# Kernel optimization log

Measured on AMD Instinct MI355X. Metric: run time of the kernel, lower is better.

## Reference

```python
import jax, jax.numpy as jnp
import numpy as np

DEPTH = 2; C = 96; DIN = 192; R = 6; N = 16; K = 4
B = 1; H0 = 64; W0 = 64; L0 = H0 * W0


def layer_norm(x, g, b, eps=1e-5):
    m = jnp.mean(x, -1, keepdims=True)
    v = jnp.var(x, -1, keepdims=True)
    return (x - m) / jnp.sqrt(v + eps) * g + b


def selective_scan(u, delta, A, Bs, Cs, D):
    # u, delta: (B, KD, L); A: (KD, N); Bs, Cs: (B, K, N, L); D: (KD,)
    Bb, KD, L = u.shape
    Kk = Bs.shape[1]; Dd = KD // Kk; Nn = A.shape[1]
    dA = jnp.exp(delta[..., None] * A[None, :, None, :])              # (B,KD,L,N)
    Bfull = jnp.broadcast_to(Bs[:, :, None], (Bb, Kk, Dd, Nn, L)).reshape(Bb, KD, Nn, L)
    Cfull = jnp.broadcast_to(Cs[:, :, None], (Bb, Kk, Dd, Nn, L)).reshape(Bb, KD, Nn, L)
    dBu = delta[..., None] * Bfull.transpose(0, 1, 3, 2) * u[..., None]  # (B,KD,L,N)
    Ct = Cfull.transpose(3, 0, 1, 2)                                   # (L,B,KD,N)

    def step(h, inp):
        dA_t, dBu_t, C_t = inp
        h = dA_t * h + dBu_t
        return h, jnp.sum(h * C_t, -1)

    init = jnp.zeros((Bb, KD, Nn), u.dtype)
    _, ys = jax.lax.scan(step, init, (dA.transpose(2, 0, 1, 3), dBu.transpose(2, 0, 1, 3), Ct))
    y = ys.transpose(1, 2, 0)                                          # (B,KD,L)
    return y + D[None, :, None] * u


def ss2d(x, in_proj_w, conv_w, conv_b, x_proj_w, dt_w, dt_b, A_logs, Ds, outn_g, outn_b, out_proj_w):
    # x: (B,H,W,C)
    Bb, H, W, Cc = x.shape
    L = H * W
    xz = x @ in_proj_w.T                                  # (B,H,W,2*DIN)
    Din = xz.shape[-1] // 2
    xc, z = xz[..., :Din], xz[..., Din:]
    xc = xc.transpose(0, 3, 1, 2)                         # (B,DIN,H,W)
    xc = jax.lax.conv_general_dilated(xc, conv_w, (1, 1), 'SAME',
                                      feature_group_count=Din,
                                      dimension_numbers=('NCHW', 'OIHW', 'NCHW'))
    xc = jax.nn.silu(xc + conv_b[None, :, None, None])
    # cross-scan: 4 directions
    x0 = xc.reshape(Bb, Din, L)
    x1 = xc.transpose(0, 1, 3, 2).reshape(Bb, Din, L)
    xs = jnp.stack([x0, x1, jnp.flip(x0, -1), jnp.flip(x1, -1)], 1)  # (B,K,DIN,L)
    x_dbl = jnp.einsum('bkdl,kcd->bkcl', xs, x_proj_w)
    dts, Bm, Cm = x_dbl[:, :, :R], x_dbl[:, :, R:R + N], x_dbl[:, :, R + N:]
    dts = jnp.einsum('bkrl,kdr->bkdl', dts, dt_w)
    u = xs.reshape(Bb, K * Din, L)
    delta = jax.nn.softplus(dts.reshape(Bb, K * Din, L) + dt_b.reshape(K * Din)[None, :, None])
    A = -jnp.exp(A_logs)                                  # (K*DIN, N)
    ys = selective_scan(u, delta, A, Bm, Cm, Ds).reshape(Bb, K, Din, L)
    # cross-merge
    y0 = ys[:, 0]
    y1 = ys[:, 1].reshape(Bb, Din, W, H).transpose(0, 1, 3, 2).reshape(Bb, Din, L)
    y2 = jnp.flip(ys[:, 2], -1)
    y3 = jnp.flip(ys[:, 3], -1).reshape(Bb, Din, W, H).transpose(0, 1, 3, 2).reshape(Bb, Din, L)
    y = (y0 + y1 + y2 + y3).transpose(0, 2, 1).reshape(Bb, H, W, Din)
    y = layer_norm(y, outn_g, outn_b)
    y = y * jax.nn.silu(z)
    return y @ out_proj_w.T                               # (B,H,W,C)


def setup_inputs() -> dict:
    key = jax.random.key(0)
    ks = jax.random.split(key, 10)
    f = jnp.float32
    rn = lambda k, s: jax.random.normal(k, s, f) * 0.02
    return {
        'x': jax.random.normal(ks[0], (B, L0, C), f),
        'H': H0, 'W': W0,
        'norm1_g': jnp.ones((DEPTH, C), f), 'norm1_b': jnp.zeros((DEPTH, C), f),
        'vssn_g': jnp.ones((DEPTH, C), f), 'vssn_b': jnp.zeros((DEPTH, C), f),
        'in_proj_w': rn(ks[1], (DEPTH, 2 * DIN, C)),
        'conv_w': rn(ks[2], (DEPTH, DIN, 1, 3, 3)),
        'conv_b': jnp.zeros((DEPTH, DIN), f),
        'x_proj_w': rn(ks[3], (DEPTH, K, R + 2 * N, DIN)),
        'dt_w': rn(ks[4], (DEPTH, K, DIN, R)),
        'dt_b': jax.random.uniform(ks[5], (DEPTH, K, DIN), f, -4.0, -2.0),
        'A_logs': jnp.log(jnp.broadcast_to(jnp.arange(1, N + 1, dtype=f), (DEPTH, K * DIN, N))),
        'Ds': jnp.ones((DEPTH, K * DIN), f),
        'outn_g': jnp.ones((DEPTH, DIN), f), 'outn_b': jnp.zeros((DEPTH, DIN), f),
        'out_proj_w': rn(ks[6], (DEPTH, C, DIN)),
        'res_conv_w': rn(ks[7], (C, C, 3, 3)),
        'res_conv_b': jnp.zeros((C,), f),
    }


def reference(x, H, W, norm1_g, norm1_b, vssn_g, vssn_b, in_proj_w, conv_w, conv_b,
              x_proj_w, dt_w, dt_b, A_logs, Ds, outn_g, outn_b, out_proj_w,
              res_conv_w, res_conv_b):
    Bb, Ll, Cc = x.shape
    shortcut = x
    for i in range(DEPTH):
        sc = x
        xn = layer_norm(x, norm1_g[i], norm1_b[i]).reshape(Bb, H, W, Cc)
        # VSSBlock: internal pre-norm + residual around SS2D (drop_path = 0)
        xi = xn + ss2d(layer_norm(xn, vssn_g[i], vssn_b[i]), in_proj_w[i], conv_w[i],
                       conv_b[i], x_proj_w[i], dt_w[i], dt_b[i], A_logs[i], Ds[i],
                       outn_g[i], outn_b[i], out_proj_w[i])
        x = sc + xi.reshape(Bb, Ll, Cc)
    xc = x.transpose(0, 2, 1).reshape(Bb, Cc, H, W)
    xc = jax.lax.conv_general_dilated(xc, res_conv_w, (1, 1), 'SAME',
                                      dimension_numbers=('NCHW', 'OIHW', 'NCHW'))
    xc = xc + res_conv_b[None, :, None, None]
    return xc.reshape(Bb, Cc, Ll).transpose(0, 2, 1) + shortcut
```

## Files before the change

kernel.cpp:

```cpp
#include <hip/hip_runtime.h>
#include <math.h>

#define LTOK 4096
#define CCH  96
#define DIN_ 192
#define KDIR 4
#define NST  16
#define KD_  768

#define O_XN     0
#define O_XZ     786432
#define O_XCONV  2359296
#define O_XCONVT 3145728
#define O_DELTA  3932160
#define O_BM     7077888
#define O_CM     7340032
#define O_YS     9961472
#define O_XCUR   13107200

__device__ __forceinline__ float siluf(float x) { return x / (1.f + __expf(-x)); }

__global__ void fusedA_kernel(const float* __restrict__ x, const float* __restrict__ g1,
                              const float* __restrict__ b1, const float* __restrict__ g2,
                              const float* __restrict__ b2, const float* __restrict__ w,
                              float* __restrict__ xn, float* __restrict__ xz) {
  __shared__ float As[96 * 72];
  __shared__ float Bs[96 * 68];
  int tid = threadIdx.x;
  int l0 = blockIdx.x * 64;
  int j0 = blockIdx.y * 64;
  int m = tid >> 2, j = tid & 3;
  int l = l0 + m;
  float v[24];
  float s = 0.f, ss = 0.f;
#pragma unroll
  for (int t = 0; t < 24; ++t) {
    int k = j + 4 * t;
    float vv = x[l * 96 + k];
    v[t] = vv; s += vv; ss += vv * vv;
  }
  s += __shfl_xor(s, 1); ss += __shfl_xor(ss, 1);
  s += __shfl_xor(s, 2); ss += __shfl_xor(ss, 2);
  float m1 = s * (1.f / 96.f);
  float rs1 = rsqrtf(ss * (1.f / 96.f) - m1 * m1 + 1e-5f);
  float s2 = 0.f, ss2 = 0.f;
#pragma unroll
  for (int t = 0; t < 24; ++t) {
    int k = j + 4 * t;
    float nv = (v[t] - m1) * rs1 * g1[k] + b1[k];
    v[t] = nv; s2 += nv; ss2 += nv * nv;
    if (blockIdx.y == 0) xn[l * 96 + k] = nv;
  }
  s2 += __shfl_xor(s2, 1); ss2 += __shfl_xor(ss2, 1);
  s2 += __shfl_xor(s2, 2); ss2 += __shfl_xor(ss2, 2);
  float m2 = s2 * (1.f / 96.f);
  float rs2 = rsqrtf(ss2 * (1.f / 96.f) - m2 * m2 + 1e-5f);
#pragma unroll
  for (int t = 0; t < 24; ++t) {
    int k = j + 4 * t;
    As[k * 72 + m] = (v[t] - m2) * rs2 * g2[k] + b2[k];
  }
  for (int qi = tid; qi < 64 * 24; qi += 256) {
    int nn = qi / 24, q = qi % 24;
    const float4 wv = *(const float4*)&w[(j0 + nn) * 96 + q * 4];
    Bs[(q * 4 + 0) * 68 + nn] = wv.x;
    Bs[(q * 4 + 1) * 68 + nn] = wv.y;
    Bs[(q * 4 + 2) * 68 + nn] = wv.z;
    Bs[(q * 4 + 3) * 68 + nn] = wv.w;
  }
  __syncthreads();
  int mg = tid & 15, ng = tid >> 4;
  float acc[4][4] = {};
  for (int k = 0; k < 96; ++k) {
    float a0 = As[k * 72 + 4 * mg + 0], a1 = As[k * 72 + 4 * mg + 1];
    float a2 = As[k * 72 + 4 * mg + 2], a3 = As[k * 72 + 4 * mg + 3];
    float b0 = Bs[k * 68 + 4 * ng + 0], b1_ = Bs[k * 68 + 4 * ng + 1];
    float b2_ = Bs[k * 68 + 4 * ng + 2], b3 = Bs[k * 68 + 4 * ng + 3];
    acc[0][0] += a0 * b0; acc[0][1] += a0 * b1_; acc[0][2] += a0 * b2_; acc[0][3] += a0 * b3;
    acc[1][0] += a1 * b0; acc[1][1] += a1 * b1_; acc[1][2] += a1 * b2_; acc[1][3] += a1 * b3;
    acc[2][0] += a2 * b0; acc[2][1] += a2 * b1_; acc[2][2] += a2 * b2_; acc[2][3] += a2 * b3;
    acc[3][0] += a3 * b0; acc[3][1] += a3 * b1_; acc[3][2] += a3 * b2_; acc[3][3] += a3 * b3;
  }
#pragma unroll
  for (int i = 0; i < 4; ++i) {
    float4 o = make_float4(acc[i][0], acc[i][1], acc[i][2], acc[i][3]);
    *(float4*)&xz[(l0 + 4 * mg + i) * 384 + j0 + 4 * ng] = o;
  }
}

__global__ void dwconvT_kernel(const float* __restrict__ xz, const float* __restrict__ cw,
                               const float* __restrict__ cb, float* __restrict__ xconv,
                               float* __restrict__ xconvT) {
  int w0 = blockIdx.x * 16, h0 = blockIdx.y * 16, d0 = blockIdx.z * 8;
  __shared__ float xs[324 * 9];
  int tid = threadIdx.x;
  for (int idx = tid; idx < 324 * 8; idx += 256) {
    int dd = idx & 7;
    int p = idx >> 3;
    int ph = p / 18, pw = p - ph * 18;
    int hh = h0 + ph - 1, ww = w0 + pw - 1;
    float v = 0.f;
    if (hh >= 0 && hh < 64 && ww >= 0 && ww < 64) v = xz[(hh * 64 + ww) * 384 + d0 + dd];
    xs[p * 9 + dd] = v;
  }
  __syncthreads();
  int wi = tid & 15, hi = tid >> 4;
  for (int dd = 0; dd < 8; ++dd) {
    int d = d0 + dd;
    float acc = cb[d];
    const float* wgt = cw + d * 9;
#pragma unroll
    for (int r = 0; r < 3; ++r)
#pragma unroll
      for (int c = 0; c < 3; ++c)
        acc += xs[((hi + r) * 18 + wi + c) * 9 + dd] * wgt[r * 3 + c];
    float o = siluf(acc);
    xconv[d * LTOK + (h0 + hi) * 64 + w0 + wi] = o;
    xconvT[d * LTOK + (w0 + wi) * 64 + h0 + hi] = o;
  }
}

__global__ __launch_bounds__(256) void projdelta_kernel(
    const float* __restrict__ xconv, const float* __restrict__ xconvT,
    const float* __restrict__ xpw, const float* __restrict__ dtw,
    const float* __restrict__ dtb, float* __restrict__ delta,
    float* __restrict__ Bm, float* __restrict__ Cm) {
  int chunk = blockIdx.x;
  int k = blockIdx.y;
  int l0 = chunk * 32;
  bool rev = (k >= 2);
  int lnat0 = rev ? (4064 - l0) : l0;
  const float* ub = ((k & 1) ? xconvT : xconv);
  __shared__ float Us[192 * 34];
  __shared__ float Ws[38 * 196];
  __shared__ float xdm[6 * 34];
  int tid = threadIdx.x;
  for (int idx = tid; idx < 192 * 8; idx += 256) {
    int q = idx & 7, d = idx >> 3;
    float4 v = *(const float4*)&ub[d * LTOK + lnat0 + 4 * q];
    *(float4*)&Us[d * 34 + 4 * q] = v;
  }
  for (int idx = tid; idx < 38 * 48; idx += 256) {
    int q = idx % 48, c = idx / 48;
    float4 v = *(const float4*)&xpw[(k * 38 + c) * 192 + 4 * q];
    *(float4*)&Ws[c * 196 + 4 * q] = v;
  }
  __syncthreads();
  int ip = tid & 31;
  int cg = tid >> 5;
  int crow[5];
#pragma unroll
  for (int j = 0; j < 5; ++j) {
    int c = cg * 5 + j;
    crow[j] = ((c < 38) ? c : 0) * 196;
  }
  float acc[5] = {};
  for (int d = 0; d < 192; d += 4) {
    float u0 = Us[(d + 0) * 34 + ip];
    float u1 = Us[(d + 1) * 34 + ip];
    float u2 = Us[(d + 2) * 34 + ip];
    float u3 = Us[(d + 3) * 34 + ip];
#pragma unroll
    for (int j = 0; j < 5; ++j) {
      const float4 wv = *(const float4*)&Ws[crow[j] + d];
      acc[j] += u0 * wv.x + u1 * wv.y + u2 * wv.z + u3 * wv.w;
    }
  }
  int i = rev ? (31 - ip) : ip;
  int l = l0 + i;
#pragma unroll
  for (int j = 0; j < 5; ++j) {
    int c = cg * 5 + j;
    if (c < 6)       xdm[c * 34 + ip] = acc[j];
    else if (c < 22) Bm[((k << 12) + l) * NST + (c - 6)] = acc[j];
    else if (c < 38) Cm[((k << 12) + l) * NST + (c - 22)] = acc[j];
  }
  __syncthreads();
  const float* dtwk = dtw + k * 192 * 6;
  const float* dtbk = dtb + k * 192;
  int dg = tid >> 5;
  for (int m = 0; m < 24; ++m) {
    int d = dg + 8 * m;
    float a = dtbk[d];
#pragma unroll
    for (int r = 0; r < 6; ++r) a += dtwk[d * 6 + r] * xdm[r * 34 + ip];
    float sp = (a > 20.f) ? a : log1pf(__expf(a));
    delta[(k * 192 + d) * LTOK + l] = sp;
  }
}

__global__ __launch_bounds__(512) void scan_fused(
    const float* __restrict__ delta, const float* __restrict__ Bm,
    const float* __restrict__ Cm, const float* __restrict__ xconv,
    const float* __restrict__ xconvT, const float* __restrict__ A_logs,
    const float* __restrict__ Ds, float* __restrict__ ys) {
  int kd = blockIdx.x;
  int k = kd / 192, d = kd - k * 192;
  int tid = threadIdx.x;
  int nq = tid & 3;
  int c = tid >> 2;
  const float* ub = ((k & 1) ? xconvT : xconv) + d * LTOK;
  bool rev = (k >= 2);
  float A0 = -__expf(A_logs[kd * 16 + 4 * nq + 0]);
  float A1 = -__expf(A_logs[kd * 16 + 4 * nq + 1]);
  float A2 = -__expf(A_logs[kd * 16 + 4 * nq + 2]);
  float A3 = -__expf(A_logs[kd * 16 + 4 * nq + 3]);
  const float* dp = delta + kd * LTOK;
  const float* bp = Bm + k * LTOK * NST;
  const float* cp = Cm + k * LTOK * NST;
  __shared__ float Ps[16 * 132], Qs[16 * 132], H0s[16 * 132];
  int l0 = c * 32;
  float h0 = 0.f, h1 = 0.f, h2 = 0.f, h3 = 0.f;
  float P0 = 1.f, P1 = 1.f, P2 = 1.f, P3 = 1.f;
  for (int t = 0; t < 32; t += 4) {
    int l = l0 + t;
    float4 dlt4 = *(const float4*)(dp + l);
    float4 u4;
    if (!rev) u4 = *(const float4*)(ub + l);
    else { float4 tp = *(const float4*)(ub + 4092 - l); u4 = make_float4(tp.w, tp.z, tp.y, tp.x); }
#pragma unroll
    for (int s = 0; s < 4; ++s) {
      float dlt = (s == 0) ? dlt4.x : (s == 1) ? dlt4.y : (s == 2) ? dlt4.z : dlt4.w;
      float uu  = (s == 0) ? u4.x  : (s == 1) ? u4.y  : (s == 2) ? u4.z  : u4.w;
      float4 B4 = *(const float4*)(bp + (l + s) * NST + 4 * nq);
      float du = dlt * uu;
      float a0 = __expf(dlt * A0), a1 = __expf(dlt * A1);
      float a2 = __expf(dlt * A2), a3 = __expf(dlt * A3);
      h0 = a0 * h0 + du * B4.x; h1 = a1 * h1 + du * B4.y;
      h2 = a2 * h2 + du * B4.z; h3 = a3 * h3 + du * B4.w;
      P0 *= a0; P1 *= a1; P2 *= a2; P3 *= a3;
    }
  }
  Ps[(4 * nq + 0) * 132 + c] = P0; Qs[(4 * nq + 0) * 132 + c] = h0;
  Ps[(4 * nq + 1) * 132 + c] = P1; Qs[(4 * nq + 1) * 132 + c] = h1;
  Ps[(4 * nq + 2) * 132 + c] = P2; Qs[(4 * nq + 2) * 132 + c] = h2;
  Ps[(4 * nq + 3) * 132 + c] = P3; Qs[(4 * nq + 3) * 132 + c] = h3;
  __syncthreads();
  {
    int wv = tid >> 6, lane = tid & 63;
#pragma unroll
    for (int r = 0; r < 2; ++r) {
      int nn = wv * 2 + r;
      float P = Ps[nn * 132 + lane];
      float S = Qs[nn * 132 + lane];
#pragma unroll
      for (int off = 1; off < 64; off <<= 1) {
        float pp = __shfl_up(P, off);
        float sp = __shfl_up(S, off);
        if (lane >= off) { S = sp * P + S; P = pp * P; }
      }
      float g0 = __shfl_up(S, 1);
      if (lane == 0) g0 = 0.f;
      H0s[nn * 132 + lane] = g0;
      float T0 = __shfl(S, 63);
      float P1_ = Ps[nn * 132 + 64 + lane];
      float S1_ = Qs[nn * 132 + 64 + lane];
#pragma unroll
      for (int off = 1; off < 64; off <<= 1) {
        float pp = __shfl_up(P1_, off);
        float sp = __shfl_up(S1_, off);
        if (lane >= off) { S1_ = sp * P1_ + S1_; P1_ = pp * P1_; }
      }
      float gex = __shfl_up(S1_, 1);
      float pex = __shfl_up(P1_, 1);
      if (lane == 0) { gex = 0.f; pex = 1.f; }
      H0s[nn * 132 + 64 + lane] = pex * T0 + gex;
    }
  }
  __syncthreads();
  float Dv = Ds[kd];
  float* yk = ys + (k * DIN_ + d) * LTOK;
  h0 = H0s[(4 * nq + 0) * 132 + c];
  h1 = H0s[(4 * nq + 1) * 132 + c];
  h2 = H0s[(4 * nq + 2) * 132 + c];
  h3 = H0s[(4 * nq + 3) * 132 + c];
  int row1 = 32 * (c & 1);
  int col1 = c >> 1;
  for (int t = 0; t < 32; t += 4) {
    int l = l0 + t;
    float4 dlt4 = *(const float4*)(dp + l);
    float4 u4;
    if (!rev) u4 = *(const float4*)(ub + l);
    else { float4 tp = *(const float4*)(ub + 4092 - l); u4 = make_float4(tp.w, tp.z, tp.y, tp.x); }
    float y4[4];
#pragma unroll
    for (int s = 0; s < 4; ++s) {
      float dlt = (s == 0) ? dlt4.x : (s == 1) ? dlt4.y : (s == 2) ? dlt4.z : dlt4.w;
      float uu  = (s == 0) ? u4.x  : (s == 1) ? u4.y  : (s == 2) ? u4.z  : u4.w;
      float4 B4 = *(const float4*)(bp + (l + s) * NST + 4 * nq);
      float4 C4 = *(const float4*)(cp + (l + s) * NST + 4 * nq);
      float du = dlt * uu;
      float a0 = __expf(dlt * A0), a1 = __expf(dlt * A1);
      float a2 = __expf(dlt * A2), a3 = __expf(dlt * A3);
      h0 = a0 * h0 + du * B4.x; h1 = a1 * h1 + du * B4.y;
      h2 = a2 * h2 + du * B4.z; h3 = a3 * h3 + du * B4.w;
      float p = h0 * C4.x + h1 * C4.y + h2 * C4.z + h3 * C4.w;
      p += __shfl_xor(p, 1);
      p += __shfl_xor(p, 2);
      y4[s] = p + Dv * uu;
    }
    if (nq == 0) {
      if (k == 0) {
        *(float4*)(yk + l) = make_float4(y4[0], y4[1], y4[2], y4[3]);
      } else if (k == 2) {
        *(float4*)(yk + 4092 - l) = make_float4(y4[3], y4[2], y4[1], y4[0]);
      } else if (k == 1) {
#pragma unroll
        for (int s = 0; s < 4; ++s) yk[(row1 + t + s) * 64 + col1] = y4[s];
      } else {
#pragma unroll
        for (int s = 0; s < 4; ++s) yk[(63 - row1 - (t + s)) * 64 + (63 - col1)] = y4[s];
      }
    }
  }
}

__global__ void combine_out(const float* __restrict__ ys, const float* __restrict__ xz,
                            const float* __restrict__ xn, const float* __restrict__ xsrc,
                            const float* __restrict__ og, const float* __restrict__ ob,
                            const float* __restrict__ ow, float* __restrict__ xout) {
  __shared__ float Ys[192 * 33];
  __shared__ float Bs[64 * 100];
  int tid = threadIdx.x;
  int l0 = blockIdx.x * 32;
  for (int it = tid; it < 192 * 8; it += 256) {
    int d = it >> 3, g = it & 7;
    int l = l0 + g * 4;
    float4 a0 = *(const float4*)&ys[(0 * DIN_ + d) * LTOK + l];
    float4 a1 = *(const float4*)&ys[(1 * DIN_ + d) * LTOK + l];
    float4 a2 = *(const float4*)&ys[(2 * DIN_ + d) * LTOK + l];
    float4 a3 = *(const float4*)&ys[(3 * DIN_ + d) * LTOK + l];
    float* yr = &Ys[d * 33 + g * 4];
    yr[0] = a0.x + a1.x + a2.x + a3.x;
    yr[1] = a0.y + a1.y + a2.y + a3.y;
    yr[2] = a0.z + a1.z + a2.z + a3.z;
    yr[3] = a0.w + a1.w + a2.w + a3.w;
  }
  __syncthreads();
  {
    int m = tid >> 3, q = tid & 7;
    int l = l0 + m;
    float zval[24];
    const float* zp = xz + l * 384 + 192 + q * 24;
#pragma unroll
    for (int i = 0; i < 6; ++i) {
      float4 zv = *(const float4*)(zp + 4 * i);
      zval[4 * i + 0] = zv.x; zval[4 * i + 1] = zv.y;
      zval[4 * i + 2] = zv.z; zval[4 * i + 3] = zv.w;
    }
    float s = 0.f, ssum = 0.f;
    float vv[24];
#pragma unroll
    for (int i = 0; i < 24; ++i) {
      float v = Ys[(q * 24 + i) * 33 + m];
      vv[i] = v; s += v; ssum += v * v;
    }
    s += __shfl_xor(s, 1); ssum += __shfl_xor(ssum, 1);
    s += __shfl_xor(s, 2); ssum += __shfl_xor(ssum, 2);
    s += __shfl_xor(s, 4); ssum += __shfl_xor(ssum, 4);
    float mu = s * (1.f / 192.f);
    float rs = rsqrtf(ssum * (1.f / 192.f) - mu * mu + 1e-5f);
#pragma unroll
    for (int i = 0; i < 24; ++i) {
      int d = q * 24 + i;
      float yn = (vv[i] - mu) * rs * og[d] + ob[d];
      Ys[d * 33 + m] = yn * siluf(zval[i]);
    }
  }
  int mg = tid & 31, cg = tid >> 5;
  float acc[12] = {};
  for (int kc = 0; kc < 3; ++kc) {
    __syncthreads();
    for (int qi = tid; qi < 96 * 16; qi += 256) {
      int cix = qi / 16, q = qi % 16;
      const float4 wv = *(const float4*)&ow[cix * 192 + kc * 64 + q * 4];
      Bs[(q * 4 + 0) * 100 + cix] = wv.x;
      Bs[(q * 4 + 1) * 100 + cix] = wv.y;
      Bs[(q * 4 + 2) * 100 + cix] = wv.z;
      Bs[(q * 4 + 3) * 100 + cix] = wv.w;
    }
    __syncthreads();
    for (int kk = 0; kk < 64; ++kk) {
      float a = Ys[(kc * 64 + kk) * 33 + mg];
      const float* br = &Bs[kk * 100 + cg * 12];
#pragma unroll
      for (int jj = 0; jj < 12; ++jj) acc[jj] += a * br[jj];
    }
  }
  int ll = l0 + mg;
#pragma unroll
  for (int jj = 0; jj < 12; ++jj) {
    int cix = cg * 12 + jj;
    xout[ll * 96 + cix] = xsrc[ll * 96 + cix] + xn[ll * 96 + cix] + acc[jj];
  }
}

__global__ void resconv_part(const float* __restrict__ x, const float* __restrict__ w,
                             float* __restrict__ pbuf) {
  int tile = blockIdx.x;
  int cs = blockIdx.y;
  int th0 = (tile >> 3) * 8, tw0 = (tile & 7) * 8;
  int cbase = cs * 6;
  __shared__ float xs[600];
  __shared__ float wlds[96 * 6 * 12];
  int tid = threadIdx.x;
  for (int idx = tid; idx < 600; idx += 256) {
    int cc = idx % 6;
    int pos = idx / 6;
    int hh = th0 + pos / 10 - 1;
    int ww = tw0 + pos % 10 - 1;
    float v = 0.f;
    if (hh >= 0 && hh < 64 && ww >= 0 && ww < 64) v = x[(hh * 64 + ww) * 96 + cbase + cc];
    xs[cc * 100 + pos] = v;
  }
  for (int idx = tid; idx < 96 * 54; idx += 256) {
    int c0 = idx / 54, o = idx - c0 * 54;
    int cc = o / 9, t = o - cc * 9;
    wlds[(c0 * 6 + cc) * 12 + t] = w[c0 * 864 + (cbase + cc) * 9 + t];
  }
  __syncthreads();
  int lane = tid & 63;
  int th = lane >> 3, tw = lane & 7;
  int c0g = tid >> 6;
  float acc[24] = {};
  for (int cc = 0; cc < 6; ++cc) {
    float xv[9];
#pragma unroll
    for (int r = 0; r < 3; ++r)
#pragma unroll
      for (int q = 0; q < 3; ++q) xv[r * 3 + q] = xs[cc * 100 + (th + r) * 10 + tw + q];
#pragma unroll
    for (int j = 0; j < 24; ++j) {
      const float* wr = &wlds[((c0g * 24 + j) * 6 + cc) * 12];
      float4 w0 = *(const float4*)wr;
      float4 w1 = *(const float4*)(wr + 4);
      float w8 = wr[8];
      acc[j] += xv[0] * w0.x + xv[1] * w0.y + xv[2] * w0.z + xv[3] * w0.w
              + xv[4] * w1.x + xv[5] * w1.y + xv[6] * w1.z + xv[7] * w1.w + xv[8] * w8;
    }
  }
  int l = (th0 + th) * 64 + tw0 + tw;
  float* pb = pbuf + cs * 393216 + l * 96 + c0g * 24;
#pragma unroll
  for (int j = 0; j < 24; j += 4)
    *(float4*)(pb + j) = make_float4(acc[j], acc[j + 1], acc[j + 2], acc[j + 3]);
}

__global__ void resconv_reduce(const float* __restrict__ pbuf, const float* __restrict__ b,
                               const float* __restrict__ shortcut, float* __restrict__ out) {
  int i4 = blockIdx.x * 256 + threadIdx.x;
  int base = i4 * 4;
  int c4 = base % 96;
  float4 s = *(const float4*)(shortcut + base);
  float4 bb = *(const float4*)(b + c4);
  s.x += bb.x; s.y += bb.y; s.z += bb.z; s.w += bb.w;
#pragma unroll
  for (int ss = 0; ss < 16; ++ss) {
    float4 p = *(const float4*)(pbuf + ss * 393216 + base);
    s.x += p.x; s.y += p.y; s.z += p.z; s.w += p.w;
  }
  *(float4*)(out + base) = s;
}

extern "C" void kernel_launch(void* const* d_in, const int* in_sizes, int n_in,
                              void* d_out, int out_size, void* d_ws, size_t ws_size,
                              hipStream_t stream) {
  const float* x_in     = (const float*)d_in[0];
  const float* norm1_g  = (const float*)d_in[3];
  const float* norm1_b  = (const float*)d_in[4];
  const float* vssn_g   = (const float*)d_in[5];
  const float* vssn_b   = (const float*)d_in[6];
  const float* in_proj  = (const float*)d_in[7];
  const float* conv_w   = (const float*)d_in[8];
  const float* conv_b   = (const float*)d_in[9];
  const float* x_proj   = (const float*)d_in[10];
  const float* dt_w     = (const float*)d_in[11];
  const float* dt_b     = (const float*)d_in[12];
  const float* A_logs   = (const float*)d_in[13];
  const float* Ds       = (const float*)d_in[14];
  const float* outn_g   = (const float*)d_in[15];
  const float* outn_b   = (const float*)d_in[16];
  const float* out_proj = (const float*)d_in[17];
  const float* rc_w     = (const float*)d_in[18];
  const float* rc_b     = (const float*)d_in[19];

  float* ws = (float*)d_ws;
  float* xn    = ws + O_XN;
  float* xz    = ws + O_XZ;
  float* xconv = ws + O_XCONV;
  float* xconvT= ws + O_XCONVT;
  float* delta = ws + O_DELTA;
  float* Bm    = ws + O_BM;
  float* Cm    = ws + O_CM;
  float* ysb   = ws + O_YS;
  float* xcur  = ws + O_XCUR;
  float* pbuf  = ws + O_DELTA;

  const float* xsrc = x_in;
  for (int i = 0; i < 2; ++i) {
    fusedA_kernel<<<dim3(64, 6), 256, 0, stream>>>(xsrc,
        norm1_g + i * 96, norm1_b + i * 96, vssn_g + i * 96, vssn_b + i * 96,
        in_proj + i * 36864, xn, xz);
    dwconvT_kernel<<<dim3(4, 4, 24), 256, 0, stream>>>(xz, conv_w + i * 1728,
        conv_b + i * 192, xconv, xconvT);
    projdelta_kernel<<<dim3(128, 4), 256, 0, stream>>>(xconv, xconvT,
        x_proj + i * 29184, dt_w + i * 4608, dt_b + i * 768, delta, Bm, Cm);
    scan_fused<<<768, 512, 0, stream>>>(delta, Bm, Cm, xconv, xconvT,
        A_logs + i * 12288, Ds + i * 768, ysb);
    combine_out<<<128, 256, 0, stream>>>(ysb, xz, xn, xsrc,
        outn_g + i * 192, outn_b + i * 192, out_proj + i * 18432, xcur);
    xsrc = xcur;
  }
  resconv_part<<<dim3(64, 16), 256, 0, stream>>>(xcur, rc_w, pbuf);
  resconv_reduce<<<384, 256, 0, stream>>>(pbuf, rc_b, x_in, (float*)d_out);
}
```

Measured before the change: 355.9 us.

## Accumulate four-direction scan outputs with atomics and shrink combine tile

```diff
diff --git a/kernel.cpp b/kernel.cpp
--- a/kernel.cpp
+++ b/kernel.cpp
@@ -193,7 +193,7 @@
     const float* __restrict__ delta, const float* __restrict__ Bm,
     const float* __restrict__ Cm, const float* __restrict__ xconv,
     const float* __restrict__ xconvT, const float* __restrict__ A_logs,
-    const float* __restrict__ Ds, float* __restrict__ ys) {
+    const float* __restrict__ Ds, float* __restrict__ ysum) {
   int kd = blockIdx.x;
   int k = kd / 192, d = kd - k * 192;
   int tid = threadIdx.x;
@@ -269,7 +269,7 @@
   }
   __syncthreads();
   float Dv = Ds[kd];
-  float* yk = ys + (k * DIN_ + d) * LTOK;
+  float* yd = ysum + d * LTOK;
   h0 = H0s[(4 * nq + 0) * 132 + c];
   h1 = H0s[(4 * nq + 1) * 132 + c];
   h2 = H0s[(4 * nq + 2) * 132 + c];
@@ -301,74 +301,70 @@
     }
     if (nq == 0) {
       if (k == 0) {
-        *(float4*)(yk + l) = make_float4(y4[0], y4[1], y4[2], y4[3]);
+#pragma unroll
+        for (int s = 0; s < 4; ++s) atomicAdd(yd + l + s, y4[s]);
       } else if (k == 2) {
-        *(float4*)(yk + 4092 - l) = make_float4(y4[3], y4[2], y4[1], y4[0]);
+#pragma unroll
+        for (int s = 0; s < 4; ++s) atomicAdd(yd + 4095 - (l + s), y4[s]);
       } else if (k == 1) {
 #pragma unroll
-        for (int s = 0; s < 4; ++s) yk[(row1 + t + s) * 64 + col1] = y4[s];
+        for (int s = 0; s < 4; ++s) atomicAdd(yd + (row1 + t + s) * 64 + col1, y4[s]);
       } else {
 #pragma unroll
-        for (int s = 0; s < 4; ++s) yk[(63 - row1 - (t + s)) * 64 + (63 - col1)] = y4[s];
+        for (int s = 0; s < 4; ++s) atomicAdd(yd + (63 - row1 - (t + s)) * 64 + (63 - col1), y4[s]);
       }
     }
   }
 }
 
-__global__ void combine_out(const float* __restrict__ ys, const float* __restrict__ xz,
+__global__ void combine_out(const float* __restrict__ ysum, const float* __restrict__ xz,
                             const float* __restrict__ xn, const float* __restrict__ xsrc,
                             const float* __restrict__ og, const float* __restrict__ ob,
                             const float* __restrict__ ow, float* __restrict__ xout) {
-  __shared__ float Ys[192 * 33];
+  __shared__ float Ys[192 * 17];
   __shared__ float Bs[64 * 100];
   int tid = threadIdx.x;
-  int l0 = blockIdx.x * 32;
-  for (int it = tid; it < 192 * 8; it += 256) {
-    int d = it >> 3, g = it & 7;
-    int l = l0 + g * 4;
-    float4 a0 = *(const float4*)&ys[(0 * DIN_ + d) * LTOK + l];
-    float4 a1 = *(const float4*)&ys[(1 * DIN_ + d) * LTOK + l];
-    float4 a2 = *(const float4*)&ys[(2 * DIN_ + d) * LTOK + l];
-    float4 a3 = *(const float4*)&ys[(3 * DIN_ + d) * LTOK + l];
-    float* yr = &Ys[d * 33 + g * 4];
-    yr[0] = a0.x + a1.x + a2.x + a3.x;
-    yr[1] = a0.y + a1.y + a2.y + a3.y;
-    yr[2] = a0.z + a1.z + a2.z + a3.z;
-    yr[3] = a0.w + a1.w + a2.w + a3.w;
+  int l0 = blockIdx.x * 16;
+  for (int it = tid; it < 192 * 4; it += 256) {
+    int d = it >> 2, g = it & 3;
+    float4 v = *(const float4*)&ysum[d * LTOK + l0 + g * 4];
+    float* yr = &Ys[d * 17 + g * 4];
+    yr[0] = v.x; yr[1] = v.y; yr[2] = v.z; yr[3] = v.w;
   }
   __syncthreads();
   {
-    int m = tid >> 3, q = tid & 7;
+    int m = tid >> 4, q = tid & 15;
     int l = l0 + m;
-    float zval[24];
-    const float* zp = xz + l * 384 + 192 + q * 24;
-#pragma unroll
-    for (int i = 0; i < 6; ++i) {
+    float zval[12];
+    const float* zp = xz + l * 384 + 192 + q * 12;
+#pragma unroll
+    for (int i = 0; i < 3; ++i) {
       float4 zv = *(const float4*)(zp + 4 * i);
       zval[4 * i + 0] = zv.x; zval[4 * i + 1] = zv.y;
       zval[4 * i + 2] = zv.z; zval[4 * i + 3] = zv.w;
     }
     float s = 0.f, ssum = 0.f;
-    float vv[24];
-#pragma unroll
-    for (int i = 0; i < 24; ++i) {
-      float v = Ys[(q * 24 + i) * 33 + m];
+    float vv[12];
+#pragma unroll
+    for (int i = 0; i < 12; ++i) {
+      float v = Ys[(q * 12 + i) * 17 + m];
       vv[i] = v; s += v; ssum += v * v;
     }
     s += __shfl_xor(s, 1); ssum += __shfl_xor(ssum, 1);
     s += __shfl_xor(s, 2); ssum += __shfl_xor(ssum, 2);
     s += __shfl_xor(s, 4); ssum += __shfl_xor(ssum, 4);
+    s += __shfl_xor(s, 8); ssum += __shfl_xor(ssum, 8);
     float mu = s * (1.f / 192.f);
     float rs = rsqrtf(ssum * (1.f / 192.f) - mu * mu + 1e-5f);
 #pragma unroll
-    for (int i = 0; i < 24; ++i) {
-      int d = q * 24 + i;
+    for (int i = 0; i < 12; ++i) {
+      int d = q * 12 + i;
       float yn = (vv[i] - mu) * rs * og[d] + ob[d];
-      Ys[d * 33 + m] = yn * siluf(zval[i]);
-    }
-  }
-  int mg = tid & 31, cg = tid >> 5;
-  float acc[12] = {};
+      Ys[d * 17 + m] = yn * siluf(zval[i]);
+    }
+  }
+  int mg = tid & 15, cg = tid >> 4;
+  float acc[6] = {};
   for (int kc = 0; kc < 3; ++kc) {
     __syncthreads();
     for (int qi = tid; qi < 96 * 16; qi += 256) {
@@ -381,16 +377,16 @@
     }
     __syncthreads();
     for (int kk = 0; kk < 64; ++kk) {
-      float a = Ys[(kc * 64 + kk) * 33 + mg];
-      const float* br = &Bs[kk * 100 + cg * 12];
-#pragma unroll
-      for (int jj = 0; jj < 12; ++jj) acc[jj] += a * br[jj];
+      float a = Ys[(kc * 64 + kk) * 17 + mg];
+      const float* br = &Bs[kk * 100 + cg * 6];
+#pragma unroll
+      for (int jj = 0; jj < 6; ++jj) acc[jj] += a * br[jj];
     }
   }
   int ll = l0 + mg;
 #pragma unroll
-  for (int jj = 0; jj < 12; ++jj) {
-    int cix = cg * 12 + jj;
+  for (int jj = 0; jj < 6; ++jj) {
+    int cix = cg * 6 + jj;
     xout[ll * 96 + cix] = xsrc[ll * 96 + cix] + xn[ll * 96 + cix] + acc[jj];
   }
 }
@@ -492,7 +488,7 @@
   float* delta = ws + O_DELTA;
   float* Bm    = ws + O_BM;
   float* Cm    = ws + O_CM;
-  float* ysb   = ws + O_YS;
+  float* ysum  = ws + O_YS;
   float* xcur  = ws + O_XCUR;
   float* pbuf  = ws + O_DELTA;
 
@@ -505,9 +501,10 @@
         conv_b + i * 192, xconv, xconvT);
     projdelta_kernel<<<dim3(128, 4), 256, 0, stream>>>(xconv, xconvT,
         x_proj + i * 29184, dt_w + i * 4608, dt_b + i * 768, delta, Bm, Cm);
+    hipMemsetAsync(ysum, 0, (size_t)DIN_ * LTOK * sizeof(float), stream);
     scan_fused<<<768, 512, 0, stream>>>(delta, Bm, Cm, xconv, xconvT,
-        A_logs + i * 12288, Ds + i * 768, ysb);
-    combine_out<<<128, 256, 0, stream>>>(ysb, xz, xn, xsrc,
+        A_logs + i * 12288, Ds + i * 768, ysum);
+    combine_out<<<256, 256, 0, stream>>>(ysum, xz, xn, xsrc,
         outn_g + i * 192, outn_b + i * 192, out_proj + i * 18432, xcur);
     xsrc = xcur;
   }
```

After: 760.5 us. 114% more time.
